# Optimization experiments

Hardware: AMD Instinct MI355X
Metric: run time of the kernel (lower is better)

Reference implementation:

```python
import jax, jax.numpy as jnp
import numpy as np
import math

C = 512
H = W = 64
B = 4
NUM_GROUPS = 32
EPS = 1e-6
NUM_HEADS = 1  # num_head_channels=None -> 1 head


def group_norm(x, scale, bias):
    # x: [B, H, W, C] -> normalize per group of channels over (H, W, group-chans)
    b, h, w, c = x.shape
    xg = x.reshape(b, h, w, NUM_GROUPS, c // NUM_GROUPS)
    mean = xg.mean(axis=(1, 2, 4), keepdims=True)
    var = xg.var(axis=(1, 2, 4), keepdims=True)
    xg = (xg - mean) * jax.lax.rsqrt(var + EPS)
    x = xg.reshape(b, h, w, c)
    return x * scale + bias


def setup_inputs() -> dict:
    key = jax.random.key(0)
    ks = jax.random.split(key, 5)
    s = 1.0 / math.sqrt(C)
    return {
        "hidden_states": jax.random.normal(ks[0], (B, H, W, C), jnp.float32),
        "gn_scale": jnp.ones((C,), jnp.float32),
        "gn_bias": jnp.zeros((C,), jnp.float32),
        "Wq": jax.random.normal(ks[1], (C, C), jnp.float32) * s,
        "bq": jnp.zeros((C,), jnp.float32),
        "Wk": jax.random.normal(ks[2], (C, C), jnp.float32) * s,
        "bk": jnp.zeros((C,), jnp.float32),
        "Wv": jax.random.normal(ks[3], (C, C), jnp.float32) * s,
        "bv": jnp.zeros((C,), jnp.float32),
        "Wp": jax.random.normal(ks[4], (C, C), jnp.float32) * s,
        "bp": jnp.zeros((C,), jnp.float32),
    }


def reference(hidden_states, gn_scale, gn_bias, Wq, bq, Wk, bk, Wv, bv, Wp, bp):
    residual = hidden_states
    b, h, w, c = hidden_states.shape
    x = group_norm(hidden_states, gn_scale, gn_bias)
    x = x.reshape(b, h * w, c)  # [B, N, C]

    hd = c // NUM_HEADS
    def heads(t):  # [B, N, C] -> [B, nh, N, hd]
        return t.reshape(b, h * w, NUM_HEADS, hd).transpose(0, 2, 1, 3)

    q = heads(x @ Wq + bq)
    k = heads(x @ Wk + bk)
    v = heads(x @ Wv + bv)

    scale = 1.0 / math.sqrt(math.sqrt(c / NUM_HEADS))
    attn = jnp.einsum('bhqc,bhkc->bhqk', q * scale, k * scale)
    attn = jax.nn.softmax(attn, axis=-1)
    out = jnp.einsum('bhkc,bhqk->bhqc', v, attn)  # [B, nh, N, hd]
    out = out.transpose(0, 2, 1, 3).reshape(b, h * w, c)
    out = out @ Wp + bp
    out = out.reshape(b, h, w, c)
    return out + residual
```

## Files before the change

kernel.cpp:

```cpp
#include <hip/hip_runtime.h>
#include <hip/hip_bf16.h>

typedef __attribute__((ext_vector_type(8))) short bf16x8;
typedef __attribute__((ext_vector_type(4))) float f32x4;
typedef __attribute__((ext_vector_type(4))) unsigned short u16x4;

#define MFMA16(a, b, c) __builtin_amdgcn_mfma_f32_16x16x32_bf16(a, b, c, 0, 0, 0)

#define SCALE 0.21022410381342865f

__device__ __forceinline__ unsigned short f2bf(float f) {
    union { float f; unsigned u; } v; v.f = f;
    unsigned r = v.u + 0x7FFF + ((v.u >> 16) & 1);
    return (unsigned short)(r >> 16);
}

__device__ __forceinline__ unsigned cvtpk(float lo, float hi) {
    unsigned r;
    asm("v_cvt_pk_bf16_f32 %0, %1, %2" : "=v"(r) : "v"(lo), "v"(hi));
    return r;
}

typedef __attribute__((address_space(3))) void lds_void;
typedef const __attribute__((address_space(1))) void gbl_void;
__device__ __forceinline__ void g2l16(const void* g, void* l) {
    __builtin_amdgcn_global_load_lds((gbl_void*)g, (lds_void*)l, 16, 0, 0);
}

#define PHASE_BARRIER() do { \
    asm volatile("s_waitcnt vmcnt(0) lgkmcnt(0)" ::: "memory"); \
    __builtin_amdgcn_s_barrier(); \
    __builtin_amdgcn_sched_barrier(0); \
} while (0)

#define LGKM_BARRIER() do { \
    asm volatile("s_waitcnt lgkmcnt(0)" ::: "memory"); \
    __builtin_amdgcn_s_barrier(); \
    __builtin_amdgcn_sched_barrier(0); \
} while (0)

__global__ __launch_bounds__(256) void gn_kernel(
    const float* __restrict__ x, const float* __restrict__ gamma,
    const float* __restrict__ beta, unsigned short* __restrict__ xn)
{
    int b = blockIdx.x >> 5, g = blockIdx.x & 31;
    int t = threadIdx.x;
    const float4* xf4 = (const float4*)x;
    size_t base4 = (size_t)b * (4096 * 128) + g * 4;

    float s = 0.f, ss = 0.f;
    for (int i = 0; i < 64; ++i) {
        int flat = i * 256 + t;
        int hw = flat >> 2, c4 = flat & 3;
        float4 v = xf4[base4 + (size_t)hw * 128 + c4];
        s  += v.x + v.y + v.z + v.w;
        ss += v.x * v.x + v.y * v.y + v.z * v.z + v.w * v.w;
    }
    for (int m = 32; m >= 1; m >>= 1) { s += __shfl_xor(s, m); ss += __shfl_xor(ss, m); }
    __shared__ float rs_[4], rss_[4];
    int wv = t >> 6;
    if ((t & 63) == 0) { rs_[wv] = s; rss_[wv] = ss; }
    __syncthreads();
    float tot  = rs_[0] + rs_[1] + rs_[2] + rs_[3];
    float tot2 = rss_[0] + rss_[1] + rss_[2] + rss_[3];
    float mean = tot * (1.f / 65536.f);
    float var  = tot2 * (1.f / 65536.f) - mean * mean;
    float rstd = rsqrtf(var + 1e-6f);

    const float4* g4 = (const float4*)gamma;
    const float4* b4 = (const float4*)beta;
    for (int i = 0; i < 64; ++i) {
        int flat = i * 256 + t;
        int hw = flat >> 2, c4 = flat & 3;
        float4 v  = xf4[base4 + (size_t)hw * 128 + c4];
        float4 gm = g4[g * 4 + c4], bt = b4[g * 4 + c4];
        u16x4 o;
        o.x = f2bf((v.x - mean) * rstd * gm.x + bt.x);
        o.y = f2bf((v.y - mean) * rstd * gm.y + bt.y);
        o.z = f2bf((v.z - mean) * rstd * gm.z + bt.z);
        o.w = f2bf((v.w - mean) * rstd * gm.w + bt.w);
        size_t m_ = (size_t)(b * 4096 + hw);
        *(u16x4*)&xn[m_ * 512 + g * 16 + c4 * 4] = o;
    }
}

__global__ __launch_bounds__(256) void wprep(
    const float* __restrict__ Wq, const float* __restrict__ Wk,
    const float* __restrict__ Wv, const float* __restrict__ Wp,
    unsigned short* __restrict__ wqkvt, unsigned short* __restrict__ wpt)
{
    int idx = blockIdx.x * 256 + threadIdx.x;
    if (idx < 786432) {
        int n = idx >> 9, k = idx & 511;
        int j = n >> 9, nn = n & 511;
        const float* W = (j == 0) ? Wq : (j == 1) ? Wk : Wv;
        wqkvt[idx] = f2bf(W[k * 512 + nn]);
    } else {
        int i2 = idx - 786432;
        int n = i2 >> 9, k = i2 & 511;
        wpt[i2] = f2bf(Wp[k * 512 + n]);
    }
}

template <int MODE>
__global__ __launch_bounds__(256) void gemm_kernel(
    const unsigned short* __restrict__ A, const unsigned short* __restrict__ Bt,
    const float* __restrict__ bias_q, const float* __restrict__ bias_k,
    const float* __restrict__ bias_v, const float* __restrict__ bias_p,
    const float* __restrict__ resid,
    unsigned short* __restrict__ Cbf, float* __restrict__ Cf)
{
    const int K = 512;
    int m0 = blockIdx.x * 128;
    int n0 = blockIdx.y * 128;
    int t = threadIdx.x;
    int l = t & 63, w = t >> 6;
    int wm = w >> 1, wn = w & 1;
    int lr = l & 15, lg = l >> 4;

    __shared__ unsigned short As[128][72];
    __shared__ unsigned short Bs[128][72];

    f32x4 acc[4][4];
    for (int i = 0; i < 4; ++i)
        for (int j = 0; j < 4; ++j) acc[i][j] = f32x4{0.f, 0.f, 0.f, 0.f};

    for (int k0 = 0; k0 < K; k0 += 64) {
        for (int c = 0; c < 4; ++c) {
            int flat = c * 256 + t;
            int row = flat >> 3, kc = (flat & 7) * 8;
            *(bf16x8*)&As[row][kc] = *(const bf16x8*)&A[(size_t)(m0 + row) * K + k0 + kc];
            *(bf16x8*)&Bs[row][kc] = *(const bf16x8*)&Bt[(size_t)(n0 + row) * K + k0 + kc];
        }
        __syncthreads();
        for (int ks = 0; ks < 2; ++ks) {
            bf16x8 af[4], bfr[4];
            for (int mi = 0; mi < 4; ++mi)
                af[mi] = *(bf16x8*)&As[wm * 64 + mi * 16 + lr][ks * 32 + lg * 8];
            for (int ni = 0; ni < 4; ++ni)
                bfr[ni] = *(bf16x8*)&Bs[wn * 64 + ni * 16 + lr][ks * 32 + lg * 8];
            for (int mi = 0; mi < 4; ++mi)
                for (int ni = 0; ni < 4; ++ni)
                    acc[mi][ni] = MFMA16(af[mi], bfr[ni], acc[mi][ni]);
        }
        __syncthreads();
    }

    for (int mi = 0; mi < 4; ++mi)
        for (int ni = 0; ni < 4; ++ni)
            for (int r = 0; r < 4; ++r) {
                int row = m0 + wm * 64 + mi * 16 + lg * 4 + r;
                int col = n0 + wn * 64 + ni * 16 + lr;
                float val = acc[mi][ni][r];
                if (MODE == 0) {
                    float bias, scl;
                    if (col < 512)       { bias = bias_q[col];        scl = SCALE; }
                    else if (col < 1024) { bias = bias_k[col - 512];  scl = SCALE; }
                    else                 { bias = bias_v[col - 1024]; scl = 1.0f;  }
                    Cbf[(size_t)row * 1536 + col] = f2bf((val + bias) * scl);
                } else {
                    Cf[(size_t)row * 512 + col] =
                        val + bias_p[col] + resid[(size_t)row * 512 + col];
                }
            }
}

__global__ __launch_bounds__(256) void vtrans(
    const unsigned short* __restrict__ qkv, unsigned short* __restrict__ vT)
{
    int n0 = blockIdx.x * 64, d0 = blockIdx.y * 64, b = blockIdx.z;
    int t = threadIdx.x;
    __shared__ unsigned short tile[64][72];
    for (int c = 0; c < 2; ++c) {
        int flat = c * 256 + t;
        int r = flat >> 3, cc = (flat & 7) * 8;
        *(bf16x8*)&tile[r][cc] =
            *(const bf16x8*)&qkv[(size_t)(b * 4096 + n0 + r) * 1536 + 1024 + d0 + cc];
    }
    __syncthreads();
    for (int c = 0; c < 2; ++c) {
        int flat = c * 256 + t;
        int dr = flat >> 3, nc = (flat & 7) * 8;
        bf16x8 v;
        for (int j = 0; j < 8; ++j) v[j] = (short)tile[nc + j][dr];
        *(bf16x8*)&vT[((size_t)b * 512 + d0 + dr) * 4096 + n0 + nc] = v;
    }
}

__global__ __launch_bounds__(256, 3) void qk_kernel(
    const unsigned short* __restrict__ qkv, unsigned short* __restrict__ P,
    float* __restrict__ lpart, int b0)
{
    int W = blockIdx.x;
    int xcd = W & 7, i = W >> 3;
    int bb = xcd >> 2;
    int nb = (xcd & 3) * 8 + (i & 7);
    int mb = i >> 3;
    int m0 = mb * 128, n0 = nb * 128;
    int b = b0 + bb;

    int t = threadIdx.x, l = t & 63, w = t >> 6;
    int wm = w >> 1, wn = w & 1;
    int lr = l & 15, lg = l >> 4;

    __shared__ __align__(16) unsigned short lds[16896];
    unsigned short* As = lds;
    unsigned short* Bs = lds + 8192;
    float* Lw = (float*)(lds + 16384);

    const unsigned short* A_ = qkv + (size_t)(b * 4096 + m0) * 1536 + 512;
    const unsigned short* B_ = qkv + (size_t)(b * 4096 + n0) * 1536;

    auto stage = [&](int s) {
        int k0 = s * 64;
#pragma unroll
        for (int c = 0; c < 4; ++c) {
            int flat = c * 256 + t;
            int row = flat >> 3, u = flat & 7;
            g2l16(A_ + (size_t)row * 1536 + k0 + ((u ^ (row & 7)) << 3),
                  As + (flat << 3));
        }
#pragma unroll
        for (int c = 0; c < 4; ++c) {
            int flat = c * 256 + t;
            int row = flat >> 3, u = flat & 7;
            g2l16(B_ + (size_t)row * 1536 + k0 + ((u ^ (row & 7)) << 3),
                  Bs + (flat << 3));
        }
    };

    f32x4 acc[4][4];
#pragma unroll
    for (int mi = 0; mi < 4; ++mi)
#pragma unroll
        for (int ni = 0; ni < 4; ++ni) acc[mi][ni] = f32x4{0.f, 0.f, 0.f, 0.f};

    for (int s = 0; s < 8; ++s) {
        if (s) LGKM_BARRIER();
        stage(s);
        PHASE_BARRIER();
        __builtin_amdgcn_s_setprio(1);
#pragma unroll
        for (int ks = 0; ks < 2; ++ks) {
            bf16x8 af[4], bfr[4];
#pragma unroll
            for (int mi = 0; mi < 4; ++mi) {
                int row = wm * 64 + mi * 16 + lr;
                af[mi] = *(const bf16x8*)&As[(row * 8 + ((ks * 4 + lg) ^ (row & 7))) << 3];
            }
#pragma unroll
            for (int ni = 0; ni < 4; ++ni) {
                int row = wn * 64 + ni * 16 + lr;
                bfr[ni] = *(const bf16x8*)&Bs[(row * 8 + ((ks * 4 + lg) ^ (row & 7))) << 3];
            }
#pragma unroll
            for (int mi = 0; mi < 4; ++mi)
#pragma unroll
                for (int ni = 0; ni < 4; ++ni)
                    acc[mi][ni] = MFMA16(af[mi], bfr[ni], acc[mi][ni]);
        }
        __builtin_amdgcn_s_setprio(0);
    }
    LGKM_BARRIER();

    unsigned short* Pl = lds;
    {
        float sums[4] = {0.f, 0.f, 0.f, 0.f};
#pragma unroll
        for (int mi = 0; mi < 4; ++mi) {
            int u = wm * 8 + mi * 2 + (lg >> 1);
            int half = lg & 1;
#pragma unroll
            for (int ni = 0; ni < 4; ++ni) {
                float p0 = __expf(acc[mi][ni][0]);
                float p1 = __expf(acc[mi][ni][1]);
                float p2 = __expf(acc[mi][ni][2]);
                float p3 = __expf(acc[mi][ni][3]);
                sums[ni] += p0 + p1 + p2 + p3;
                int q = wn * 64 + ni * 16 + lr;
                unsigned* dst = (unsigned*)&((char*)Pl)[
                    q * 256 + ((u ^ (q & 7)) << 4) + (half << 3)];
                dst[0] = cvtpk(p0, p1);
                dst[1] = cvtpk(p2, p3);
            }
        }
#pragma unroll
        for (int ni = 0; ni < 4; ++ni) {
            float v = sums[ni];
            v += __shfl_xor(v, 16);
            v += __shfl_xor(v, 32);
            if (lg == 0) Lw[wm * 128 + wn * 64 + ni * 16 + lr] = v;
        }
    }
    LGKM_BARRIER();

    if (t < 128)
        lpart[(size_t)(bb * 32 + mb) * 4096 + n0 + t] = Lw[t] + Lw[128 + t];

#pragma unroll
    for (int c = 0; c < 8; ++c) {
        int flat = c * 256 + t;
        int row = flat >> 4, u = flat & 15;
        *(bf16x8*)&P[((size_t)(bb * 4096 + n0 + row)) * 4096 + m0 + u * 8] =
            *(const bf16x8*)&((char*)Pl)[row * 256 + ((u ^ (row & 7)) << 4)];
    }
}

__global__ __launch_bounds__(256) void lred_kernel(
    const float* __restrict__ lpart, float* __restrict__ lsum)
{
    int rr = blockIdx.x * 256 + threadIdx.x;
    int bb = rr >> 12, r = rr & 4095;
    float s = 0.f;
#pragma unroll
    for (int sl = 0; sl < 32; ++sl)
        s += lpart[(size_t)(bb * 32 + sl) * 4096 + r];
    lsum[rr] = 1.0f / s;
}

__global__ __launch_bounds__(512) void pv_kernel(
    const unsigned short* __restrict__ P, const unsigned short* __restrict__ vT,
    const float* __restrict__ linv, unsigned short* __restrict__ outb, int b0)
{
    int m0 = blockIdx.x * 128, n0 = blockIdx.y * 128, bb = blockIdx.z;
    int b = b0 + bb;
    int t = threadIdx.x, l = t & 63, w = t >> 6;
    int wm = w >> 2, wn = w & 3;
    int lr = l & 15, lg = l >> 4;

    __shared__ __align__(16) unsigned short lds[49152];
    unsigned short* As = lds;
    unsigned short* Bs = lds + 24576;

    const unsigned short* A_ = P + (size_t)(bb * 4096 + m0) * 4096;
    const unsigned short* B_ = vT + ((size_t)b * 512 + n0) * 4096;

    auto stage = [&](int s, int buf) {
        int k0 = s * 64;
        unsigned short* ad = As + buf * 8192;
        unsigned short* bd = Bs + buf * 8192;
#pragma unroll
        for (int c = 0; c < 2; ++c) {
            int flat = c * 512 + t;
            int row = flat >> 3, u = flat & 7;
            g2l16(A_ + (size_t)row * 4096 + k0 + ((u ^ (row & 7)) << 3),
                  ad + (flat << 3));
        }
#pragma unroll
        for (int c = 0; c < 2; ++c) {
            int flat = c * 512 + t;
            int row = flat >> 3, u = flat & 7;
            g2l16(B_ + (size_t)row * 4096 + k0 + ((u ^ (row & 7)) << 3),
                  bd + (flat << 3));
        }
    };

    f32x4 acc[4][2];
#pragma unroll
    for (int i = 0; i < 4; ++i)
#pragma unroll
        for (int j = 0; j < 2; ++j) acc[i][j] = f32x4{0.f, 0.f, 0.f, 0.f};

    stage(0, 0);
    stage(1, 1);
    asm volatile("s_waitcnt vmcnt(4)" ::: "memory");
    __builtin_amdgcn_s_barrier();
    __builtin_amdgcn_sched_barrier(0);

    for (int s = 0; s < 64; ++s) {
        if (s + 2 < 64) stage(s + 2, (s + 2) % 3);
        const unsigned short* Al = As + (s % 3) * 8192;
        const unsigned short* Bl = Bs + (s % 3) * 8192;
        __builtin_amdgcn_s_setprio(1);
#pragma unroll
        for (int ks = 0; ks < 2; ++ks) {
            bf16x8 af[4], bfr[2];
#pragma unroll
            for (int mi = 0; mi < 4; ++mi) {
                int row = wm * 64 + mi * 16 + lr;
                af[mi] = *(const bf16x8*)&Al[(row * 8 + ((ks * 4 + lg) ^ (row & 7))) << 3];
            }
#pragma unroll
            for (int ni = 0; ni < 2; ++ni) {
                int row = wn * 32 + ni * 16 + lr;
                bfr[ni] = *(const bf16x8*)&Bl[(row * 8 + ((ks * 4 + lg) ^ (row & 7))) << 3];
            }
#pragma unroll
            for (int mi = 0; mi < 4; ++mi)
#pragma unroll
                for (int ni = 0; ni < 2; ++ni)
                    acc[mi][ni] = MFMA16(af[mi], bfr[ni], acc[mi][ni]);
        }
        __builtin_amdgcn_s_setprio(0);
        if (s < 62) asm volatile("s_waitcnt vmcnt(4) lgkmcnt(0)" ::: "memory");
        else        asm volatile("s_waitcnt vmcnt(0) lgkmcnt(0)" ::: "memory");
        __builtin_amdgcn_s_barrier();
        __builtin_amdgcn_sched_barrier(0);
    }

#pragma unroll
    for (int mi = 0; mi < 4; ++mi)
#pragma unroll
        for (int r = 0; r < 4; ++r) {
            int row = m0 + wm * 64 + mi * 16 + lg * 4 + r;
            float inv = linv[bb * 4096 + row];
#pragma unroll
            for (int ni = 0; ni < 2; ++ni) {
                int col = n0 + wn * 32 + ni * 16 + lr;
                outb[(size_t)(b * 4096 + row) * 512 + col] =
                    f2bf(acc[mi][ni][r] * inv);
            }
        }
}

extern "C" void kernel_launch(void* const* d_in, const int* in_sizes, int n_in,
                              void* d_out, int out_size, void* d_ws, size_t ws_size,
                              hipStream_t stream)
{
    const float* x     = (const float*)d_in[0];
    const float* gamma = (const float*)d_in[1];
    const float* beta  = (const float*)d_in[2];
    const float* Wq = (const float*)d_in[3];
    const float* bq = (const float*)d_in[4];
    const float* Wk = (const float*)d_in[5];
    const float* bk = (const float*)d_in[6];
    const float* Wv = (const float*)d_in[7];
    const float* bv = (const float*)d_in[8];
    const float* Wp = (const float*)d_in[9];
    const float* bp = (const float*)d_in[10];
    float* out = (float*)d_out;

    unsigned short* xn    = (unsigned short*)d_ws;
    unsigned short* wqkvt = xn + (size_t)16384 * 512;
    unsigned short* wpt   = wqkvt + (size_t)1536 * 512;
    unsigned short* qkv   = wpt + (size_t)512 * 512;
    unsigned short* vT    = qkv + (size_t)16384 * 1536;
    unsigned short* P     = vT + (size_t)4 * 512 * 4096;
    float* lpart = (float*)(P + (size_t)2 * 4096 * 4096);
    float* linv  = lpart + (size_t)128 * 4096;

    gn_kernel<<<dim3(128), dim3(256), 0, stream>>>(x, gamma, beta, xn);
    wprep<<<dim3(4096), dim3(256), 0, stream>>>(Wq, Wk, Wv, Wp, wqkvt, wpt);
    gemm_kernel<0><<<dim3(128, 12), dim3(256), 0, stream>>>(
        xn, wqkvt, bq, bk, bv, nullptr, nullptr, qkv, nullptr);
    vtrans<<<dim3(64, 8, 4), dim3(256), 0, stream>>>(qkv, vT);

    for (int b0 = 0; b0 < 4; b0 += 2) {
        qk_kernel<<<dim3(2048), dim3(256), 0, stream>>>(qkv, P, lpart, b0);
        lred_kernel<<<dim3(32), dim3(256), 0, stream>>>(lpart, linv);
        pv_kernel<<<dim3(32, 4, 2), dim3(512), 0, stream>>>(P, vT, linv, xn, b0);
    }

    gemm_kernel<1><<<dim3(128, 4), dim3(256), 0, stream>>>(
        xn, wpt, nullptr, nullptr, nullptr, bp, x, nullptr, out);
}
```

Before: 284.3 us.

## Split group norm into parallel stats/apply kernels and use direct-to-LDS swizzled GEMM loads

The single 128-block group-norm kernel becomes a 1024-block partial-statistics kernel and a 2048-block apply kernel, so the memory-bound pass can use the whole GPU instead of a few blocks. The QKV/projection GEMM now loads tiles with global_load_lds into an XOR-swizzled unpadded LDS layout, raises wave priority during MFMA, and sets an occupancy hint of three blocks. This trades one extra launch and a small stats buffer for parallelism, and relies on the swizzle being bank-conflict free.

```diff
diff --git a/kernel.cpp b/kernel.cpp
--- a/kernel.cpp
+++ b/kernel.cpp
@@ -39,19 +39,21 @@
     __builtin_amdgcn_sched_barrier(0); \
 } while (0)
 
-__global__ __launch_bounds__(256) void gn_kernel(
-    const float* __restrict__ x, const float* __restrict__ gamma,
-    const float* __restrict__ beta, unsigned short* __restrict__ xn)
-{
-    int b = blockIdx.x >> 5, g = blockIdx.x & 31;
+__global__ __launch_bounds__(256) void gn_stats(
+    const float* __restrict__ x, float2* __restrict__ gstats)
+{
+    int id = blockIdx.x;
+    int b = id >> 8, rem = id & 255;
+    int g = rem >> 3, sl = rem & 7;
     int t = threadIdx.x;
     const float4* xf4 = (const float4*)x;
     size_t base4 = (size_t)b * (4096 * 128) + g * 4;
 
     float s = 0.f, ss = 0.f;
-    for (int i = 0; i < 64; ++i) {
+#pragma unroll
+    for (int i = 0; i < 8; ++i) {
         int flat = i * 256 + t;
-        int hw = flat >> 2, c4 = flat & 3;
+        int hw = sl * 512 + (flat >> 2), c4 = flat & 3;
         float4 v = xf4[base4 + (size_t)hw * 128 + c4];
         s  += v.x + v.y + v.z + v.w;
         ss += v.x * v.x + v.y * v.y + v.z * v.z + v.w * v.w;
@@ -61,17 +63,42 @@
     int wv = t >> 6;
     if ((t & 63) == 0) { rs_[wv] = s; rss_[wv] = ss; }
     __syncthreads();
-    float tot  = rs_[0] + rs_[1] + rs_[2] + rs_[3];
-    float tot2 = rss_[0] + rss_[1] + rss_[2] + rss_[3];
-    float mean = tot * (1.f / 65536.f);
-    float var  = tot2 * (1.f / 65536.f) - mean * mean;
+    if (t == 0) {
+        float2 o;
+        o.x = rs_[0] + rs_[1] + rs_[2] + rs_[3];
+        o.y = rss_[0] + rss_[1] + rss_[2] + rss_[3];
+        gstats[id] = o;
+    }
+}
+
+__global__ __launch_bounds__(256) void gn_apply(
+    const float* __restrict__ x, const float* __restrict__ gamma,
+    const float* __restrict__ beta, const float2* __restrict__ gstats,
+    unsigned short* __restrict__ xn)
+{
+    int id = blockIdx.x;
+    int b = id >> 9, rem = id & 511;
+    int g = rem >> 4, sl = rem & 15;
+    int t = threadIdx.x;
+
+    float s = 0.f, ss = 0.f;
+#pragma unroll
+    for (int i = 0; i < 8; ++i) {
+        float2 p = gstats[(b * 32 + g) * 8 + i];
+        s += p.x; ss += p.y;
+    }
+    float mean = s * (1.f / 65536.f);
+    float var  = ss * (1.f / 65536.f) - mean * mean;
     float rstd = rsqrtf(var + 1e-6f);
 
+    const float4* xf4 = (const float4*)x;
     const float4* g4 = (const float4*)gamma;
     const float4* b4 = (const float4*)beta;
-    for (int i = 0; i < 64; ++i) {
+    size_t base4 = (size_t)b * (4096 * 128) + g * 4;
+#pragma unroll
+    for (int i = 0; i < 4; ++i) {
         int flat = i * 256 + t;
-        int hw = flat >> 2, c4 = flat & 3;
+        int hw = sl * 256 + (flat >> 2), c4 = flat & 3;
         float4 v  = xf4[base4 + (size_t)hw * 128 + c4];
         float4 gm = g4[g * 4 + c4], bt = b4[g * 4 + c4];
         u16x4 o;
@@ -79,8 +106,7 @@
         o.y = f2bf((v.y - mean) * rstd * gm.y + bt.y);
         o.z = f2bf((v.z - mean) * rstd * gm.z + bt.z);
         o.w = f2bf((v.w - mean) * rstd * gm.w + bt.w);
-        size_t m_ = (size_t)(b * 4096 + hw);
-        *(u16x4*)&xn[m_ * 512 + g * 16 + c4 * 4] = o;
+        *(u16x4*)&xn[(size_t)(b * 4096 + hw) * 512 + g * 16 + c4 * 4] = o;
     }
 }
 
@@ -103,14 +129,13 @@
 }
 
 template <int MODE>
-__global__ __launch_bounds__(256) void gemm_kernel(
+__global__ __launch_bounds__(256, 3) void gemm_kernel(
     const unsigned short* __restrict__ A, const unsigned short* __restrict__ Bt,
     const float* __restrict__ bias_q, const float* __restrict__ bias_k,
     const float* __restrict__ bias_v, const float* __restrict__ bias_p,
     const float* __restrict__ resid,
     unsigned short* __restrict__ Cbf, float* __restrict__ Cf)
 {
-    const int K = 512;
     int m0 = blockIdx.x * 128;
     int n0 = blockIdx.y * 128;
     int t = threadIdx.x;
@@ -118,36 +143,69 @@
     int wm = w >> 1, wn = w & 1;
     int lr = l & 15, lg = l >> 4;
 
-    __shared__ unsigned short As[128][72];
-    __shared__ unsigned short Bs[128][72];
-
-    f32x4 acc[4][4];
-    for (int i = 0; i < 4; ++i)
-        for (int j = 0; j < 4; ++j) acc[i][j] = f32x4{0.f, 0.f, 0.f, 0.f};
-
-    for (int k0 = 0; k0 < K; k0 += 64) {
+    __shared__ __align__(16) unsigned short lds[16384];
+    unsigned short* As = lds;
+    unsigned short* Bs = lds + 8192;
+
+    const unsigned short* A_ = A + (size_t)m0 * 512;
+    const unsigned short* B_ = Bt + (size_t)n0 * 512;
+
+    auto stage = [&](int s) {
+        int k0 = s * 64;
+#pragma unroll
         for (int c = 0; c < 4; ++c) {
             int flat = c * 256 + t;
-            int row = flat >> 3, kc = (flat & 7) * 8;
-            *(bf16x8*)&As[row][kc] = *(const bf16x8*)&A[(size_t)(m0 + row) * K + k0 + kc];
-            *(bf16x8*)&Bs[row][kc] = *(const bf16x8*)&Bt[(size_t)(n0 + row) * K + k0 + kc];
-        }
-        __syncthreads();
+            int row = flat >> 3, u = flat & 7;
+            g2l16(A_ + (size_t)row * 512 + k0 + ((u ^ (row & 7)) << 3),
+                  As + (flat << 3));
+        }
+#pragma unroll
+        for (int c = 0; c < 4; ++c) {
+            int flat = c * 256 + t;
+            int row = flat >> 3, u = flat & 7;
+            g2l16(B_ + (size_t)row * 512 + k0 + ((u ^ (row & 7)) << 3),
+                  Bs + (flat << 3));
+        }
+    };
+
+    f32x4 acc[4][4];
+#pragma unroll
+    for (int i = 0; i < 4; ++i)
+#pragma unroll
+        for (int j = 0; j < 4; ++j) acc[i][j] = f32x4{0.f, 0.f, 0.f, 0.f};
+
+    for (int s = 0; s < 8; ++s) {
+        if (s) LGKM_BARRIER();
+        stage(s);
+        PHASE_BARRIER();
+        __builtin_amdgcn_s_setprio(1);
+#pragma unroll
         for (int ks = 0; ks < 2; ++ks) {
             bf16x8 af[4], bfr[4];
+#pragma unroll
+            for (int mi = 0; mi < 4; ++mi) {
+                int row = wm * 64 + mi * 16 + lr;
+                af[mi] = *(const bf16x8*)&As[(row * 8 + ((ks * 4 + lg) ^ (row & 7))) << 3];
+            }
+#pragma unroll
+            for (int ni = 0; ni < 4; ++ni) {
+                int row = wn * 64 + ni * 16 + lr;
+                bfr[ni] = *(const bf16x8*)&Bs[(row * 8 + ((ks * 4 + lg) ^ (row & 7))) << 3];
+            }
+#pragma unroll
             for (int mi = 0; mi < 4; ++mi)
-                af[mi] = *(bf16x8*)&As[wm * 64 + mi * 16 + lr][ks * 32 + lg * 8];
-            for (int ni = 0; ni < 4; ++ni)
-                bfr[ni] = *(bf16x8*)&Bs[wn * 64 + ni * 16 + lr][ks * 32 + lg * 8];
-            for (int mi = 0; mi < 4; ++mi)
+#pragma unroll
                 for (int ni = 0; ni < 4; ++ni)
                     acc[mi][ni] = MFMA16(af[mi], bfr[ni], acc[mi][ni]);
         }
-        __syncthreads();
-    }
-
+        __builtin_amdgcn_s_setprio(0);
+    }
+
+#pragma unroll
     for (int mi = 0; mi < 4; ++mi)
+#pragma unroll
         for (int ni = 0; ni < 4; ++ni)
+#pragma unroll
             for (int r = 0; r < 4; ++r) {
                 int row = m0 + wm * 64 + mi * 16 + lg * 4 + r;
                 int col = n0 + wn * 64 + ni * 16 + lr;
@@ -438,8 +496,10 @@
     unsigned short* P     = vT + (size_t)4 * 512 * 4096;
     float* lpart = (float*)(P + (size_t)2 * 4096 * 4096);
     float* linv  = lpart + (size_t)128 * 4096;
-
-    gn_kernel<<<dim3(128), dim3(256), 0, stream>>>(x, gamma, beta, xn);
+    float2* gstats = (float2*)(linv + 8192);
+
+    gn_stats<<<dim3(1024), dim3(256), 0, stream>>>(x, gstats);
+    gn_apply<<<dim3(2048), dim3(256), 0, stream>>>(x, gamma, beta, gstats, xn);
     wprep<<<dim3(4096), dim3(256), 0, stream>>>(Wq, Wk, Wv, Wp, wqkvt, wpt);
     gemm_kernel<0><<<dim3(128, 12), dim3(256), 0, stream>>>(
         xn, wqkvt, bq, bk, bv, nullptr, nullptr, qkv, nullptr);
```

Measured after the change: 252.8 us. 1.12x faster.
